# Kernel optimization log

Measured on AMD Instinct MI355X. Metric: run time of the kernel, lower is better.

The kernel has to match this reference:

```python
import jax, jax.numpy as jnp
import numpy as np

T, B, H = 1024, 16, 1024
S = 2048


def setup_inputs() -> dict:
    key = jax.random.key(0)
    k1, k2, k3, k4 = jax.random.split(key, 4)
    output = jax.random.normal(k1, (T, B, H), dtype=jnp.float32)
    memory = jax.random.normal(k2, (S, B, H), dtype=jnp.float32)
    attn_mask = jnp.zeros((B, T, S), dtype=jnp.bool_)  # True = masked
    # linear_out: Linear(2H -> H); torch weight layout [out, in]
    W = jax.random.normal(k3, (H, 2 * H), dtype=jnp.float32) * (1.0 / np.sqrt(2 * H))
    b = jax.random.normal(k4, (H,), dtype=jnp.float32) * 0.01
    return {"output": output, "memory": memory, "attn_mask": attn_mask, "W": W, "b": b}


def reference(output, memory, attn_mask, W, b):
    # scores: (B, T, S) = output^T @ memory (unscaled dot product)
    attn = jnp.einsum('tbh,sbh->bts', output, memory)
    attn = jnp.where(attn_mask, -jnp.inf, attn)
    attn = jax.nn.softmax(attn, axis=2)
    # context: (T, B, H)
    context = jnp.einsum('bts,sbh->tbh', attn, memory)
    combined = jnp.concatenate([context, output], axis=2)  # (T, B, 2H)
    out = jnp.tanh(jnp.einsum('tbd,hd->tbh', combined, W) + b)
    return (out, attn)
```

## Files before the change

kernel.cpp:

```cpp
#include <hip/hip_runtime.h>
#include <hip/hip_bf16.h>
#include <math.h>

#define Tn 1024
#define Bn 16
#define Hn 1024
#define Sn 2048

typedef __attribute__((ext_vector_type(8))) short bf16x8;
typedef __attribute__((ext_vector_type(8))) unsigned short u16x8;
typedef __attribute__((ext_vector_type(4))) float f32x4;

__device__ __forceinline__ unsigned short f2bf(float x) {
  unsigned u = __float_as_uint(x);
  u += 0x7fffu + ((u >> 16) & 1u);
  return (unsigned short)(u >> 16);
}
__device__ __forceinline__ float bf2f(unsigned short h) {
  return __uint_as_float(((unsigned)h) << 16);
}

__device__ __forceinline__ void gload16(const void* g, void* l) {
  __builtin_amdgcn_global_load_lds((const __attribute__((address_space(1))) void*)g,
                                   (__attribute__((address_space(3))) void*)l, 16, 0, 0);
}

__device__ __forceinline__ int xcd_swz(int bid, int nwg) {
  return (bid & 7) * (nwg >> 3) + (bid >> 3);
}


__global__ __launch_bounds__(256) void k_split_plane(const float* __restrict__ src,
                                                     unsigned short* __restrict__ hiP,
                                                     unsigned short* __restrict__ loP,
                                                     int rows) {
  const int i = blockIdx.x * 256 + threadIdx.x;
  const int h8 = i & (Hn / 8 - 1);
  const int rem = i >> 7;
  const int b = rem & (Bn - 1);
  const int r = rem >> 4;
  const float4 a = *(const float4*)(src + (size_t)i * 8);
  const float4 c = *(const float4*)(src + (size_t)i * 8 + 4);
  const float v[8] = {a.x, a.y, a.z, a.w, c.x, c.y, c.z, c.w};
  u16x8 hv, lv;
#pragma unroll
  for (int j = 0; j < 8; ++j) {
    const unsigned short h = f2bf(v[j]);
    hv[j] = h;
    lv[j] = f2bf(v[j] - bf2f(h));
  }
  const size_t dst = ((size_t)b * rows + r) * Hn + h8 * 8;
  *(u16x8*)(hiP + dst) = hv;
  *(u16x8*)(loP + dst) = lv;
}

__global__ __launch_bounds__(256) void k_cvt8(const float* __restrict__ src,
                                              unsigned short* __restrict__ dst, int n8) {
  const int i = blockIdx.x * 256 + threadIdx.x;
  if (i >= n8) return;
  const float4 a = *(const float4*)(src + (size_t)i * 8);
  const float4 c = *(const float4*)(src + (size_t)i * 8 + 4);
  u16x8 u;
  u[0] = f2bf(a.x); u[1] = f2bf(a.y); u[2] = f2bf(a.z); u[3] = f2bf(a.w);
  u[4] = f2bf(c.x); u[5] = f2bf(c.y); u[6] = f2bf(c.z); u[7] = f2bf(c.w);
  *(u16x8*)(dst + (size_t)i * 8) = u;
}

__global__ __launch_bounds__(256) void k_trH(const unsigned short* __restrict__ memH,
                                             unsigned short* __restrict__ memT) {
  __shared__ unsigned short L[64 * 72];
  const int t = threadIdx.x;
  const int h0 = blockIdx.x * 64, s0 = blockIdx.y * 64, b = blockIdx.z;
#pragma unroll
  for (int p = 0; p < 2; ++p) {
    const int fid = p * 256 + t;
    const int s_l = fid >> 3;
    const int c = fid & 7;
    const u16x8 v = *(const u16x8*)(memH + ((size_t)b * Sn + s0 + s_l) * Hn + h0 + c * 8);
#pragma unroll
    for (int e = 0; e < 8; ++e) L[(c * 8 + e) * 72 + s_l] = v[e];
  }
  __syncthreads();
#pragma unroll
  for (int p = 0; p < 2; ++p) {
    const int cid = p * 256 + t;
    const int h_l = cid >> 3;
    const int c = cid & 7;
    const u16x8 vv = *(const u16x8*)&L[h_l * 72 + c * 8];
    *(u16x8*)(memT + ((size_t)b * Hn + h0 + h_l) * Sn + s0 + c * 8) = vv;
  }
}


__device__ __forceinline__ void stage256x64(const unsigned short* __restrict__ g, size_t ldr,
                                            unsigned short* __restrict__ lds, int tid) {
#pragma unroll
  for (int r = 0; r < 4; ++r) {
    const int row = r * 64 + (tid >> 3);
    const int cb = (tid & 7) * 16;
    const int cs = cb ^ ((row & 4) << 3);
    gload16((const char*)g + (size_t)row * ldr * 2 + cs, (char*)lds + r * 8192 + tid * 16);
  }
}

__device__ __forceinline__ void stage256x32(const unsigned short* __restrict__ g, size_t ldr,
                                            unsigned short* __restrict__ lds, int tid) {
#pragma unroll
  for (int r = 0; r < 2; ++r) {
    const int row = r * 128 + (tid >> 2);
    const int cb = (tid & 3) * 16;
    const int cs = cb ^ ((row & 8) << 2);
    gload16((const char*)g + (size_t)row * ldr * 2 + cs, (char*)lds + r * 8192 + tid * 16);
  }
}


__global__ __launch_bounds__(512, 2) void k_scores(const unsigned short* __restrict__ oH,
                                                   const unsigned short* __restrict__ oL,
                                                   const unsigned short* __restrict__ mH,
                                                   const unsigned short* __restrict__ mL,
                                                   float* __restrict__ attn) {
  __shared__ unsigned short AsH[2][256 * 32], AsL[2][256 * 32];
  __shared__ unsigned short BsH[2][256 * 32], BsL[2][256 * 32];
  const int tid = threadIdx.x, lane = tid & 63, wv = tid >> 6;
  const int wr = wv >> 2, wc = wv & 3;
  const int swz = xcd_swz(blockIdx.x, 512);
  const int bs = (swz & 7) * 256;
  const int bt = ((swz >> 3) & 3) * 256;
  const int b = swz >> 5;
  const f32x4 fz = {0.f, 0.f, 0.f, 0.f};
  f32x4 acc[8][4];
#pragma unroll
  for (int i = 0; i < 8; ++i)
#pragma unroll
    for (int j = 0; j < 4; ++j) acc[i][j] = fz;

  const unsigned short* AgH = oH + ((size_t)b * Tn + bt) * Hn;
  const unsigned short* AgL = oL + ((size_t)b * Tn + bt) * Hn;
  const unsigned short* BgH = mH + ((size_t)b * Sn + bs) * Hn;
  const unsigned short* BgL = mL + ((size_t)b * Sn + bs) * Hn;
  const int r16 = lane & 15, khB = (lane >> 4) * 16;
  const int NK = Hn / 32;

  stage256x32(AgH, Hn, AsH[0], tid);
  stage256x32(AgL, Hn, AsL[0], tid);
  stage256x32(BgH, Hn, BsH[0], tid);
  stage256x32(BgL, Hn, BsL[0], tid);

  for (int t = 0; t < NK; ++t) {
    const int cur = t & 1;
    if (t + 1 < NK) {
      const int k0 = (t + 1) * 32;
      stage256x32(AgH + k0, Hn, AsH[cur ^ 1], tid);
      stage256x32(AgL + k0, Hn, AsL[cur ^ 1], tid);
      stage256x32(BgH + k0, Hn, BsH[cur ^ 1], tid);
      stage256x32(BgL + k0, Hn, BsL[cur ^ 1], tid);
      asm volatile("s_waitcnt vmcnt(8)" ::: "memory");
    } else {
      asm volatile("s_waitcnt vmcnt(0)" ::: "memory");
    }
    __builtin_amdgcn_s_barrier();

    const char* ABh = (const char*)AsH[cur];
    const char* ABl = (const char*)AsL[cur];
    const char* BBh = (const char*)BsH[cur];
    const char* BBl = (const char*)BsL[cur];
    bf16x8 bh[2][2], bl[2][2];
#pragma unroll
    for (int nq = 0; nq < 2; ++nq)
#pragma unroll
      for (int fj = 0; fj < 2; ++fj) {
        const int rb = wc * 64 + nq * 32 + fj * 16 + r16;
        const int off = rb * 64 + (khB ^ ((rb & 8) << 2));
        bh[nq][fj] = *(const bf16x8*)(BBh + off);
        bl[nq][fj] = *(const bf16x8*)(BBl + off);
      }
#pragma unroll
    for (int mq = 0; mq < 2; ++mq) {
      bf16x8 ah[4], al[4];
#pragma unroll
      for (int fi = 0; fi < 4; ++fi) {
        const int ra = wr * 128 + mq * 64 + fi * 16 + r16;
        const int off = ra * 64 + (khB ^ ((ra & 8) << 2));
        ah[fi] = *(const bf16x8*)(ABh + off);
        al[fi] = *(const bf16x8*)(ABl + off);
      }
      __builtin_amdgcn_s_setprio(1);
#pragma unroll
      for (int nq = 0; nq < 2; ++nq)
#pragma unroll
        for (int fj = 0; fj < 2; ++fj)
#pragma unroll
          for (int fi = 0; fi < 4; ++fi) {
            f32x4& a = acc[mq * 4 + fi][nq * 2 + fj];
            a = __builtin_amdgcn_mfma_f32_16x16x32_bf16(ah[fi], bh[nq][fj], a, 0, 0, 0);
            a = __builtin_amdgcn_mfma_f32_16x16x32_bf16(ah[fi], bl[nq][fj], a, 0, 0, 0);
            a = __builtin_amdgcn_mfma_f32_16x16x32_bf16(al[fi], bh[nq][fj], a, 0, 0, 0);
          }
      __builtin_amdgcn_s_setprio(0);
    }
    __builtin_amdgcn_s_barrier();
  }
  const int rq = (lane >> 4) * 4;
  float* obase = attn + (size_t)b * Tn * Sn;
#pragma unroll
  for (int i = 0; i < 8; ++i) {
    const int m_off = wr * 128 + (i >> 2) * 64 + (i & 3) * 16;
#pragma unroll
    for (int q = 0; q < 4; ++q) {
      const int t = bt + m_off + rq + q;
#pragma unroll
      for (int j = 0; j < 4; ++j) {
        const int s = bs + wc * 64 + (j >> 1) * 32 + (j & 1) * 16 + r16;
        obase[(size_t)t * Sn + s] = acc[i][j][q];
      }
    }
  }
}


__global__ __launch_bounds__(256) void k_softmax(float* __restrict__ attn,
                                                 const unsigned char* __restrict__ mask,
                                                 unsigned short* __restrict__ attnbf) {
  const int row = blockIdx.x;
  float* p = attn + (size_t)row * Sn;
  const unsigned char* mrow = mask + (size_t)row * Sn;
  const int tid = threadIdx.x;
  const int lane = tid & 63;
  const int wv = tid >> 6;
  const float4 a = *(const float4*)(p + tid * 8);
  const float4 c = *(const float4*)(p + tid * 8 + 4);
  const unsigned long long mv = *(const unsigned long long*)(mrow + tid * 8);
  float x[8] = {a.x, a.y, a.z, a.w, c.x, c.y, c.z, c.w};
#pragma unroll
  for (int j = 0; j < 8; ++j)
    if ((mv >> (8 * j)) & 0xffull) x[j] = -INFINITY;
  float mx = x[0];
#pragma unroll
  for (int j = 1; j < 8; ++j) mx = fmaxf(mx, x[j]);
#pragma unroll
  for (int off = 32; off; off >>= 1) mx = fmaxf(mx, __shfl_xor(mx, off, 64));
  __shared__ float redmax[4], redsum[4];
  if (lane == 0) redmax[wv] = mx;
  __syncthreads();
  mx = fmaxf(fmaxf(redmax[0], redmax[1]), fmaxf(redmax[2], redmax[3]));
  float e[8];
  float s = 0.f;
#pragma unroll
  for (int j = 0; j < 8; ++j) {
    e[j] = __expf(x[j] - mx);
    s += e[j];
  }
#pragma unroll
  for (int off = 32; off; off >>= 1) s += __shfl_xor(s, off, 64);
  if (lane == 0) redsum[wv] = s;
  __syncthreads();
  s = redsum[0] + redsum[1] + redsum[2] + redsum[3];
  const float inv = 1.0f / s;
  float o[8];
#pragma unroll
  for (int j = 0; j < 8; ++j) o[j] = e[j] * inv;
  float4 o0 = {o[0], o[1], o[2], o[3]};
  float4 o1 = {o[4], o[5], o[6], o[7]};
  *(float4*)(p + tid * 8) = o0;
  *(float4*)(p + tid * 8 + 4) = o1;
  u16x8 ub;
#pragma unroll
  for (int j = 0; j < 8; ++j) ub[j] = f2bf(o[j]);
  *(u16x8*)(attnbf + (size_t)row * Sn + tid * 8) = ub;
}


__global__ __launch_bounds__(512, 2) void k_context(const unsigned short* __restrict__ attnbf,
                                                    const unsigned short* __restrict__ memT,
                                                    unsigned short* __restrict__ ctxB) {
  __shared__ unsigned short As[2][256 * 64], Bs[2][256 * 64];
  const int tid = threadIdx.x, lane = tid & 63, wv = tid >> 6;
  const int wr = wv >> 2, wc = wv & 3;
  const int swz = xcd_swz(blockIdx.x, 256);
  const int bh = (swz & 3) * 256;
  const int bt = ((swz >> 2) & 3) * 256;
  const int b = swz >> 4;
  const f32x4 fz = {0.f, 0.f, 0.f, 0.f};
  f32x4 acc[8][4];
#pragma unroll
  for (int i = 0; i < 8; ++i)
#pragma unroll
    for (int j = 0; j < 4; ++j) acc[i][j] = fz;

  const unsigned short* Ag = attnbf + ((size_t)b * Tn + bt) * Sn;
  const unsigned short* Bg = memT + ((size_t)b * Hn + bh) * Sn;
  const int r16 = lane & 15, khB = (lane >> 4) * 16;
  const int NK = Sn / 64;

  stage256x64(Ag, Sn, As[0], tid);
  stage256x64(Bg, Sn, Bs[0], tid);

  for (int t = 0; t < NK; ++t) {
    const int cur = t & 1;
    if (t + 1 < NK) {
      const int k0 = (t + 1) * 64;
      stage256x64(Ag + k0, Sn, As[cur ^ 1], tid);
      stage256x64(Bg + k0, Sn, Bs[cur ^ 1], tid);
      asm volatile("s_waitcnt vmcnt(8)" ::: "memory");
    } else {
      asm volatile("s_waitcnt vmcnt(0)" ::: "memory");
    }
    __builtin_amdgcn_s_barrier();

    const char* Ab = (const char*)As[cur];
    const char* Bb = (const char*)Bs[cur];
    bf16x8 bb[2][2][2];
#pragma unroll
    for (int nq = 0; nq < 2; ++nq)
#pragma unroll
      for (int fj = 0; fj < 2; ++fj) {
        const int rb = wc * 64 + nq * 32 + fj * 16 + r16;
#pragma unroll
        for (int ks = 0; ks < 2; ++ks) {
          const int cb = ks * 64 + khB;
          bb[nq][fj][ks] = *(const bf16x8*)(Bb + rb * 128 + (cb ^ ((rb & 4) << 3)));
        }
      }
#pragma unroll
    for (int mq = 0; mq < 2; ++mq) {
      bf16x8 aa[4][2];
#pragma unroll
      for (int fi = 0; fi < 4; ++fi) {
        const int ra = wr * 128 + mq * 64 + fi * 16 + r16;
#pragma unroll
        for (int ks = 0; ks < 2; ++ks) {
          const int cb = ks * 64 + khB;
          aa[fi][ks] = *(const bf16x8*)(Ab + ra * 128 + (cb ^ ((ra & 4) << 3)));
        }
      }
      __builtin_amdgcn_s_setprio(1);
#pragma unroll
      for (int nq = 0; nq < 2; ++nq)
#pragma unroll
        for (int fj = 0; fj < 2; ++fj)
#pragma unroll
          for (int fi = 0; fi < 4; ++fi)
#pragma unroll
            for (int ks = 0; ks < 2; ++ks) {
              f32x4& a = acc[mq * 4 + fi][nq * 2 + fj];
              a = __builtin_amdgcn_mfma_f32_16x16x32_bf16(aa[fi][ks], bb[nq][fj][ks], a, 0, 0, 0);
            }
      __builtin_amdgcn_s_setprio(0);
    }
    __builtin_amdgcn_s_barrier();
  }
  const int rq = (lane >> 4) * 4;
#pragma unroll
  for (int i = 0; i < 8; ++i) {
    const int m_off = wr * 128 + (i >> 2) * 64 + (i & 3) * 16;
#pragma unroll
    for (int q = 0; q < 4; ++q) {
      const int t = bt + m_off + rq + q;
#pragma unroll
      for (int j = 0; j < 4; ++j) {
        const int h = bh + wc * 64 + (j >> 1) * 32 + (j & 1) * 16 + r16;
        ctxB[((size_t)b * Tn + t) * Hn + h] = f2bf(acc[i][j][q]);
      }
    }
  }
}


__global__ __launch_bounds__(512, 2) void k_final(const unsigned short* __restrict__ ctxB,
                                                  const unsigned short* __restrict__ outpH,
                                                  const unsigned short* __restrict__ Wbf,
                                                  const float* __restrict__ bias,
                                                  float* __restrict__ out) {
  __shared__ unsigned short As[2][256 * 64], Bs[2][256 * 64];
  const int tid = threadIdx.x, lane = tid & 63, wv = tid >> 6;
  const int wr = wv >> 2, wc = wv & 3;
  const int swz = xcd_swz(blockIdx.x, 256);
  const int bh = (swz & 3) * 256;
  const int bm = (swz >> 2) * 256;
  const f32x4 fz = {0.f, 0.f, 0.f, 0.f};
  f32x4 acc[8][4];
#pragma unroll
  for (int i = 0; i < 8; ++i)
#pragma unroll
    for (int j = 0; j < 4; ++j) acc[i][j] = fz;

  const int r16 = lane & 15, khB = (lane >> 4) * 16;
  const int NK = (2 * Hn) / 64;
  auto Asrc = [&](int tt) -> const unsigned short* {
    return (tt < 16) ? (ctxB + (size_t)bm * Hn + tt * 64)
                     : (outpH + (size_t)bm * Hn + (tt - 16) * 64);
  };
  const unsigned short* Bg = Wbf + (size_t)bh * (2 * Hn);

  stage256x64(Asrc(0), Hn, As[0], tid);
  stage256x64(Bg, 2 * Hn, Bs[0], tid);

  for (int t = 0; t < NK; ++t) {
    const int cur = t & 1;
    if (t + 1 < NK) {
      stage256x64(Asrc(t + 1), Hn, As[cur ^ 1], tid);
      stage256x64(Bg + (t + 1) * 64, 2 * Hn, Bs[cur ^ 1], tid);
      asm volatile("s_waitcnt vmcnt(8)" ::: "memory");
    } else {
      asm volatile("s_waitcnt vmcnt(0)" ::: "memory");
    }
    __builtin_amdgcn_s_barrier();

    const char* Ab = (const char*)As[cur];
    const char* Bb = (const char*)Bs[cur];
    bf16x8 bb[2][2][2];
#pragma unroll
    for (int nq = 0; nq < 2; ++nq)
#pragma unroll
      for (int fj = 0; fj < 2; ++fj) {
        const int rb = wc * 64 + nq * 32 + fj * 16 + r16;
#pragma unroll
        for (int ks = 0; ks < 2; ++ks) {
          const int cb = ks * 64 + khB;
          bb[nq][fj][ks] = *(const bf16x8*)(Bb + rb * 128 + (cb ^ ((rb & 4) << 3)));
        }
      }
#pragma unroll
    for (int mq = 0; mq < 2; ++mq) {
      bf16x8 aa[4][2];
#pragma unroll
      for (int fi = 0; fi < 4; ++fi) {
        const int ra = wr * 128 + mq * 64 + fi * 16 + r16;
#pragma unroll
        for (int ks = 0; ks < 2; ++ks) {
          const int cb = ks * 64 + khB;
          aa[fi][ks] = *(const bf16x8*)(Ab + ra * 128 + (cb ^ ((ra & 4) << 3)));
        }
      }
      __builtin_amdgcn_s_setprio(1);
#pragma unroll
      for (int nq = 0; nq < 2; ++nq)
#pragma unroll
        for (int fj = 0; fj < 2; ++fj)
#pragma unroll
          for (int fi = 0; fi < 4; ++fi)
#pragma unroll
            for (int ks = 0; ks < 2; ++ks) {
              f32x4& a = acc[mq * 4 + fi][nq * 2 + fj];
              a = __builtin_amdgcn_mfma_f32_16x16x32_bf16(aa[fi][ks], bb[nq][fj][ks], a, 0, 0, 0);
            }
      __builtin_amdgcn_s_setprio(0);
    }
    __builtin_amdgcn_s_barrier();
  }
  const int rq = (lane >> 4) * 4;
#pragma unroll
  for (int i = 0; i < 8; ++i) {
    const int m_off = wr * 128 + (i >> 2) * 64 + (i & 3) * 16;
#pragma unroll
    for (int q = 0; q < 4; ++q) {
      const int r = bm + m_off + rq + q;
      const int b = r >> 10, t = r & (Tn - 1);
#pragma unroll
      for (int j = 0; j < 4; ++j) {
        const int h = bh + wc * 64 + (j >> 1) * 32 + (j & 1) * 16 + r16;
        out[((size_t)t * Bn + b) * Hn + h] = tanhf(acc[i][j][q] + bias[h]);
      }
    }
  }
}

extern "C" void kernel_launch(void* const* d_in, const int* in_sizes, int n_in,
                              void* d_out, int out_size, void* d_ws, size_t ws_size,
                              hipStream_t stream) {
  const float* outp = (const float*)d_in[0];
  const float* mem = (const float*)d_in[1];
  const unsigned char* mask = (const unsigned char*)d_in[2];
  const float* W = (const float*)d_in[3];
  const float* bias = (const float*)d_in[4];
  float* out = (float*)d_out;
  float* attn = out + (size_t)Tn * Bn * Hn;

  char* w = (char*)d_ws;
  unsigned short* memH  = (unsigned short*)(w);
  unsigned short* memL  = (unsigned short*)(w + ((size_t)64 << 20));
  unsigned short* outpH = (unsigned short*)(w + ((size_t)128 << 20));
  unsigned short* outpL = (unsigned short*)(w + ((size_t)160 << 20));
  unsigned short* Wbf   = (unsigned short*)(w + ((size_t)192 << 20));
  unsigned short* memT   = memL;
  unsigned short* attnbf = memH;
  unsigned short* ctxB   = outpL;

  k_split_plane<<<dim3((Tn * Bn * Hn / 8) / 256), 256, 0, stream>>>(outp, outpH, outpL, Tn);
  k_split_plane<<<dim3((Sn * Bn * Hn / 8) / 256), 256, 0, stream>>>(mem, memH, memL, Sn);
  k_cvt8<<<dim3((Hn * 2 * Hn / 8) / 256), 256, 0, stream>>>(W, Wbf, Hn * 2 * Hn / 8);

  k_scores<<<dim3(512), 512, 0, stream>>>(outpH, outpL, memH, memL, attn);
  k_trH<<<dim3(Hn / 64, Sn / 64, Bn), 256, 0, stream>>>(memH, memT);
  k_softmax<<<dim3(Bn * Tn), 256, 0, stream>>>(attn, mask, attnbf);
  k_context<<<dim3(256), 512, 0, stream>>>(attnbf, memT, ctxB);
  k_final<<<dim3(256), 512, 0, stream>>>(ctxB, outpH, Wbf, bias, out);
}
```

Before: 533.4 us.

## Interleave prefetch stages with MFMA quadrants in scores GEMM; widen LDS swizzle

The scores kernel's K-loop now splits each iteration into four quadrant sub-steps. Each sub-step loads register fragments from LDS, issues part of the next tile's global-to-LDS prefetch, and then runs that quadrant's MFMAs, so loads are spread between compute phases instead of issued in one burst. The stage256x64 swizzle changes from a single-bit XOR to a 3-bit row XOR (row&7)<<4, matching the 128-byte rows in the other two GEMMs, to cut LDS bank conflicts. The trade-off is more barriers per iteration and a full vmcnt(0) wait at the top of each iteration.

```diff
diff --git a/kernel.cpp b/kernel.cpp
--- a/kernel.cpp
+++ b/kernel.cpp
@@ -27,6 +27,10 @@
 
 __device__ __forceinline__ int xcd_swz(int bid, int nwg) {
   return (bid & 7) * (nwg >> 3) + (bid >> 3);
+}
+
+__device__ __forceinline__ f32x4 mfma16(bf16x8 a, bf16x8 b, f32x4 c) {
+  return __builtin_amdgcn_mfma_f32_16x16x32_bf16(a, b, c, 0, 0, 0);
 }
 
 
@@ -98,7 +102,7 @@
   for (int r = 0; r < 4; ++r) {
     const int row = r * 64 + (tid >> 3);
     const int cb = (tid & 7) * 16;
-    const int cs = cb ^ ((row & 4) << 3);
+    const int cs = cb ^ ((row & 7) << 4);
     gload16((const char*)g + (size_t)row * ldr * 2 + cs, (char*)lds + r * 8192 + tid * 16);
   }
 }
@@ -149,58 +153,115 @@
 
   for (int t = 0; t < NK; ++t) {
     const int cur = t & 1;
-    if (t + 1 < NK) {
-      const int k0 = (t + 1) * 32;
-      stage256x32(AgH + k0, Hn, AsH[cur ^ 1], tid);
-      stage256x32(AgL + k0, Hn, AsL[cur ^ 1], tid);
-      stage256x32(BgH + k0, Hn, BsH[cur ^ 1], tid);
-      stage256x32(BgL + k0, Hn, BsL[cur ^ 1], tid);
-      asm volatile("s_waitcnt vmcnt(8)" ::: "memory");
-    } else {
-      asm volatile("s_waitcnt vmcnt(0)" ::: "memory");
-    }
+    asm volatile("s_waitcnt vmcnt(0)" ::: "memory");
     __builtin_amdgcn_s_barrier();
 
     const char* ABh = (const char*)AsH[cur];
     const char* ABl = (const char*)AsL[cur];
     const char* BBh = (const char*)BsH[cur];
     const char* BBl = (const char*)BsL[cur];
-    bf16x8 bh[2][2], bl[2][2];
-#pragma unroll
-    for (int nq = 0; nq < 2; ++nq)
-#pragma unroll
-      for (int fj = 0; fj < 2; ++fj) {
-        const int rb = wc * 64 + nq * 32 + fj * 16 + r16;
-        const int off = rb * 64 + (khB ^ ((rb & 8) << 2));
-        bh[nq][fj] = *(const bf16x8*)(BBh + off);
-        bl[nq][fj] = *(const bf16x8*)(BBl + off);
-      }
-#pragma unroll
-    for (int mq = 0; mq < 2; ++mq) {
-      bf16x8 ah[4], al[4];
+    const int k1 = (t + 1) * 32;
+    const bool st = (t + 1) < NK;
+
+    bf16x8 ahA[4], alA[4], bhA[2], blA[2];
+#pragma unroll
+    for (int fi = 0; fi < 4; ++fi) {
+      const int ra = wr * 128 + fi * 16 + r16;
+      const int off = ra * 64 + (khB ^ ((ra & 8) << 2));
+      ahA[fi] = *(const bf16x8*)(ABh + off);
+      alA[fi] = *(const bf16x8*)(ABl + off);
+    }
+#pragma unroll
+    for (int fj = 0; fj < 2; ++fj) {
+      const int rb = wc * 64 + fj * 16 + r16;
+      const int off = rb * 64 + (khB ^ ((rb & 8) << 2));
+      bhA[fj] = *(const bf16x8*)(BBh + off);
+      blA[fj] = *(const bf16x8*)(BBl + off);
+    }
+    if (st) {
+      stage256x32(AgH + k1, Hn, AsH[cur ^ 1], tid);
+      stage256x32(AgL + k1, Hn, AsL[cur ^ 1], tid);
+    }
+    __builtin_amdgcn_s_barrier();
+    __builtin_amdgcn_s_setprio(1);
+#pragma unroll
+    for (int fj = 0; fj < 2; ++fj)
 #pragma unroll
       for (int fi = 0; fi < 4; ++fi) {
-        const int ra = wr * 128 + mq * 64 + fi * 16 + r16;
-        const int off = ra * 64 + (khB ^ ((ra & 8) << 2));
-        ah[fi] = *(const bf16x8*)(ABh + off);
-        al[fi] = *(const bf16x8*)(ABl + off);
-      }
-      __builtin_amdgcn_s_setprio(1);
-#pragma unroll
-      for (int nq = 0; nq < 2; ++nq)
-#pragma unroll
-        for (int fj = 0; fj < 2; ++fj)
-#pragma unroll
-          for (int fi = 0; fi < 4; ++fi) {
-            f32x4& a = acc[mq * 4 + fi][nq * 2 + fj];
-            a = __builtin_amdgcn_mfma_f32_16x16x32_bf16(ah[fi], bh[nq][fj], a, 0, 0, 0);
-            a = __builtin_amdgcn_mfma_f32_16x16x32_bf16(ah[fi], bl[nq][fj], a, 0, 0, 0);
-            a = __builtin_amdgcn_mfma_f32_16x16x32_bf16(al[fi], bh[nq][fj], a, 0, 0, 0);
-          }
-      __builtin_amdgcn_s_setprio(0);
-    }
-    __builtin_amdgcn_s_barrier();
-  }
+        f32x4& a = acc[fi][fj];
+        a = mfma16(ahA[fi], bhA[fj], a);
+        a = mfma16(ahA[fi], blA[fj], a);
+        a = mfma16(alA[fi], bhA[fj], a);
+      }
+    __builtin_amdgcn_s_setprio(0);
+    __builtin_amdgcn_s_barrier();
+
+    bf16x8 ahB[4], alB[4];
+#pragma unroll
+    for (int fi = 0; fi < 4; ++fi) {
+      const int ra = wr * 128 + 64 + fi * 16 + r16;
+      const int off = ra * 64 + (khB ^ ((ra & 8) << 2));
+      ahB[fi] = *(const bf16x8*)(ABh + off);
+      alB[fi] = *(const bf16x8*)(ABl + off);
+    }
+    if (st) stage256x32(BgH + k1, Hn, BsH[cur ^ 1], tid);
+    __builtin_amdgcn_s_barrier();
+    __builtin_amdgcn_s_setprio(1);
+#pragma unroll
+    for (int fj = 0; fj < 2; ++fj)
+#pragma unroll
+      for (int fi = 0; fi < 4; ++fi) {
+        f32x4& a = acc[4 + fi][fj];
+        a = mfma16(ahB[fi], bhA[fj], a);
+        a = mfma16(ahB[fi], blA[fj], a);
+        a = mfma16(alB[fi], bhA[fj], a);
+      }
+    __builtin_amdgcn_s_setprio(0);
+    __builtin_amdgcn_s_barrier();
+
+    bf16x8 bhB[2], blB[2];
+#pragma unroll
+    for (int fj = 0; fj < 2; ++fj) {
+      const int rb = wc * 64 + 32 + fj * 16 + r16;
+      const int off = rb * 64 + (khB ^ ((rb & 8) << 2));
+      bhB[fj] = *(const bf16x8*)(BBh + off);
+      blB[fj] = *(const bf16x8*)(BBl + off);
+    }
+    if (st) stage256x32(BgL + k1, Hn, BsL[cur ^ 1], tid);
+    __builtin_amdgcn_s_barrier();
+    __builtin_amdgcn_s_setprio(1);
+#pragma unroll
+    for (int fj = 0; fj < 2; ++fj)
+#pragma unroll
+      for (int fi = 0; fi < 4; ++fi) {
+        f32x4& a = acc[4 + fi][2 + fj];
+        a = mfma16(ahB[fi], bhB[fj], a);
+        a = mfma16(ahB[fi], blB[fj], a);
+        a = mfma16(alB[fi], bhB[fj], a);
+      }
+    __builtin_amdgcn_s_setprio(0);
+    __builtin_amdgcn_s_barrier();
+
+#pragma unroll
+    for (int fi = 0; fi < 4; ++fi) {
+      const int ra = wr * 128 + fi * 16 + r16;
+      const int off = ra * 64 + (khB ^ ((ra & 8) << 2));
+      ahA[fi] = *(const bf16x8*)(ABh + off);
+      alA[fi] = *(const bf16x8*)(ABl + off);
+    }
+    __builtin_amdgcn_s_setprio(1);
+#pragma unroll
+    for (int fj = 0; fj < 2; ++fj)
+#pragma unroll
+      for (int fi = 0; fi < 4; ++fi) {
+        f32x4& a = acc[fi][2 + fj];
+        a = mfma16(ahA[fi], bhB[fj], a);
+        a = mfma16(ahA[fi], blB[fj], a);
+        a = mfma16(alA[fi], bhB[fj], a);
+      }
+    __builtin_amdgcn_s_setprio(0);
+  }
+
   const int rq = (lane >> 4) * 4;
   float* obase = attn + (size_t)b * Tn * Sn;
 #pragma unroll
@@ -319,7 +380,7 @@
 #pragma unroll
         for (int ks = 0; ks < 2; ++ks) {
           const int cb = ks * 64 + khB;
-          bb[nq][fj][ks] = *(const bf16x8*)(Bb + rb * 128 + (cb ^ ((rb & 4) << 3)));
+          bb[nq][fj][ks] = *(const bf16x8*)(Bb + rb * 128 + (cb ^ ((rb & 7) << 4)));
         }
       }
 #pragma unroll
@@ -331,7 +392,7 @@
 #pragma unroll
         for (int ks = 0; ks < 2; ++ks) {
           const int cb = ks * 64 + khB;
-          aa[fi][ks] = *(const bf16x8*)(Ab + ra * 128 + (cb ^ ((ra & 4) << 3)));
+          aa[fi][ks] = *(const bf16x8*)(Ab + ra * 128 + (cb ^ ((ra & 7) << 4)));
         }
       }
       __builtin_amdgcn_s_setprio(1);
@@ -418,7 +479,7 @@
 #pragma unroll
         for (int ks = 0; ks < 2; ++ks) {
           const int cb = ks * 64 + khB;
-          bb[nq][fj][ks] = *(const bf16x8*)(Bb + rb * 128 + (cb ^ ((rb & 4) << 3)));
+          bb[nq][fj][ks] = *(const bf16x8*)(Bb + rb * 128 + (cb ^ ((rb & 7) << 4)));
         }
       }
 #pragma unroll
@@ -430,7 +491,7 @@
 #pragma unroll
         for (int ks = 0; ks < 2; ++ks) {
           const int cb = ks * 64 + khB;
-          aa[fi][ks] = *(const bf16x8*)(Ab + ra * 128 + (cb ^ ((ra & 4) << 3)));
+          aa[fi][ks] = *(const bf16x8*)(Ab + ra * 128 + (cb ^ ((ra & 7) << 4)));
         }
       }
       __builtin_amdgcn_s_setprio(1);
```

Measured after the change: 524.3 us. Within noise of the previous version (-1.7%).

## Switch scores GEMM to 32x32 MFMA and widen LDS swizzle in 64-wide stages

Applied to the files above, without the earlier changes.

The split-bf16 scores kernel now uses 32x32x16 MFMA tiles with 16-float accumulators instead of 16x16x32, which reduces fragment loads per FLOP. The K loop now waits for all outstanding loads and barriers at the top, then issues the next prefetch. This removes the trailing barrier and the partial vmcnt overlap. Separately, the 256x64 staging and the matching reads in the two other GEMMs use a 3-bit row XOR swizzle to cut LDS bank conflicts. The risks are reduced load/compute overlap and a different output store pattern.

```diff
diff --git a/kernel.cpp b/kernel.cpp
--- a/kernel.cpp
+++ b/kernel.cpp
@@ -10,6 +10,7 @@
 typedef __attribute__((ext_vector_type(8))) short bf16x8;
 typedef __attribute__((ext_vector_type(8))) unsigned short u16x8;
 typedef __attribute__((ext_vector_type(4))) float f32x4;
+typedef __attribute__((ext_vector_type(16))) float f32x16;
 
 __device__ __forceinline__ unsigned short f2bf(float x) {
   unsigned u = __float_as_uint(x);
@@ -27,6 +28,10 @@
 
 __device__ __forceinline__ int xcd_swz(int bid, int nwg) {
   return (bid & 7) * (nwg >> 3) + (bid >> 3);
+}
+
+__device__ __forceinline__ f32x16 mfma32(bf16x8 a, bf16x8 b, f32x16 c) {
+  return __builtin_amdgcn_mfma_f32_32x32x16_bf16(a, b, c, 0, 0, 0);
 }
 
 
@@ -98,7 +103,7 @@
   for (int r = 0; r < 4; ++r) {
     const int row = r * 64 + (tid >> 3);
     const int cb = (tid & 7) * 16;
-    const int cs = cb ^ ((row & 4) << 3);
+    const int cs = cb ^ ((row & 7) << 4);
     gload16((const char*)g + (size_t)row * ldr * 2 + cs, (char*)lds + r * 8192 + tid * 16);
   }
 }
@@ -128,18 +133,20 @@
   const int bs = (swz & 7) * 256;
   const int bt = ((swz >> 3) & 3) * 256;
   const int b = swz >> 5;
-  const f32x4 fz = {0.f, 0.f, 0.f, 0.f};
-  f32x4 acc[8][4];
-#pragma unroll
-  for (int i = 0; i < 8; ++i)
-#pragma unroll
-    for (int j = 0; j < 4; ++j) acc[i][j] = fz;
+  const f32x16 fz = {0.f, 0.f, 0.f, 0.f, 0.f, 0.f, 0.f, 0.f,
+                     0.f, 0.f, 0.f, 0.f, 0.f, 0.f, 0.f, 0.f};
+  f32x16 acc[4][2];
+#pragma unroll
+  for (int i = 0; i < 4; ++i)
+#pragma unroll
+    for (int j = 0; j < 2; ++j) acc[i][j] = fz;
 
   const unsigned short* AgH = oH + ((size_t)b * Tn + bt) * Hn;
   const unsigned short* AgL = oL + ((size_t)b * Tn + bt) * Hn;
   const unsigned short* BgH = mH + ((size_t)b * Sn + bs) * Hn;
   const unsigned short* BgL = mL + ((size_t)b * Sn + bs) * Hn;
-  const int r16 = lane & 15, khB = (lane >> 4) * 16;
+  const int r32 = lane & 31;
+  const int khB = (lane >> 5) * 16;
   const int NK = Hn / 32;
 
   stage256x32(AgH, Hn, AsH[0], tid);
@@ -149,73 +156,66 @@
 
   for (int t = 0; t < NK; ++t) {
     const int cur = t & 1;
+    asm volatile("s_waitcnt vmcnt(0)" ::: "memory");
+    __builtin_amdgcn_s_barrier();
+
     if (t + 1 < NK) {
-      const int k0 = (t + 1) * 32;
-      stage256x32(AgH + k0, Hn, AsH[cur ^ 1], tid);
-      stage256x32(AgL + k0, Hn, AsL[cur ^ 1], tid);
-      stage256x32(BgH + k0, Hn, BsH[cur ^ 1], tid);
-      stage256x32(BgL + k0, Hn, BsL[cur ^ 1], tid);
-      asm volatile("s_waitcnt vmcnt(8)" ::: "memory");
-    } else {
-      asm volatile("s_waitcnt vmcnt(0)" ::: "memory");
-    }
-    __builtin_amdgcn_s_barrier();
+      const int k1 = (t + 1) * 32;
+      stage256x32(AgH + k1, Hn, AsH[cur ^ 1], tid);
+      stage256x32(AgL + k1, Hn, AsL[cur ^ 1], tid);
+      stage256x32(BgH + k1, Hn, BsH[cur ^ 1], tid);
+      stage256x32(BgL + k1, Hn, BsL[cur ^ 1], tid);
+    }
 
     const char* ABh = (const char*)AsH[cur];
     const char* ABl = (const char*)AsL[cur];
     const char* BBh = (const char*)BsH[cur];
     const char* BBl = (const char*)BsL[cur];
-    bf16x8 bh[2][2], bl[2][2];
-#pragma unroll
-    for (int nq = 0; nq < 2; ++nq)
-#pragma unroll
-      for (int fj = 0; fj < 2; ++fj) {
-        const int rb = wc * 64 + nq * 32 + fj * 16 + r16;
-        const int off = rb * 64 + (khB ^ ((rb & 8) << 2));
-        bh[nq][fj] = *(const bf16x8*)(BBh + off);
-        bl[nq][fj] = *(const bf16x8*)(BBl + off);
-      }
-#pragma unroll
-    for (int mq = 0; mq < 2; ++mq) {
-      bf16x8 ah[4], al[4];
-#pragma unroll
-      for (int fi = 0; fi < 4; ++fi) {
-        const int ra = wr * 128 + mq * 64 + fi * 16 + r16;
-        const int off = ra * 64 + (khB ^ ((ra & 8) << 2));
-        ah[fi] = *(const bf16x8*)(ABh + off);
-        al[fi] = *(const bf16x8*)(ABl + off);
-      }
-      __builtin_amdgcn_s_setprio(1);
-#pragma unroll
-      for (int nq = 0; nq < 2; ++nq)
-#pragma unroll
-        for (int fj = 0; fj < 2; ++fj)
-#pragma unroll
-          for (int fi = 0; fi < 4; ++fi) {
-            f32x4& a = acc[mq * 4 + fi][nq * 2 + fj];
-            a = __builtin_amdgcn_mfma_f32_16x16x32_bf16(ah[fi], bh[nq][fj], a, 0, 0, 0);
-            a = __builtin_amdgcn_mfma_f32_16x16x32_bf16(ah[fi], bl[nq][fj], a, 0, 0, 0);
-            a = __builtin_amdgcn_mfma_f32_16x16x32_bf16(al[fi], bh[nq][fj], a, 0, 0, 0);
-          }
-      __builtin_amdgcn_s_setprio(0);
-    }
-    __builtin_amdgcn_s_barrier();
-  }
-  const int rq = (lane >> 4) * 4;
+
+    bf16x8 ah[4][2], al[4][2];
+#pragma unroll
+    for (int fi = 0; fi < 4; ++fi)
+#pragma unroll
+      for (int ks = 0; ks < 2; ++ks) {
+        const int ra = wr * 128 + fi * 32 + r32;
+        const int off = ra * 64 + ((ks * 32 + khB) ^ ((ra & 8) << 2));
+        ah[fi][ks] = *(const bf16x8*)(ABh + off);
+        al[fi][ks] = *(const bf16x8*)(ABl + off);
+      }
+#pragma unroll
+    for (int fj = 0; fj < 2; ++fj) {
+      bf16x8 bh[2], bl[2];
+#pragma unroll
+      for (int ks = 0; ks < 2; ++ks) {
+        const int rb = wc * 64 + fj * 32 + r32;
+        const int off = rb * 64 + ((ks * 32 + khB) ^ ((rb & 8) << 2));
+        bh[ks] = *(const bf16x8*)(BBh + off);
+        bl[ks] = *(const bf16x8*)(BBl + off);
+      }
+#pragma unroll
+      for (int ks = 0; ks < 2; ++ks)
+#pragma unroll
+        for (int fi = 0; fi < 4; ++fi) {
+          acc[fi][fj] = mfma32(ah[fi][ks], bh[ks], acc[fi][fj]);
+          acc[fi][fj] = mfma32(ah[fi][ks], bl[ks], acc[fi][fj]);
+          acc[fi][fj] = mfma32(al[fi][ks], bh[ks], acc[fi][fj]);
+        }
+    }
+  }
+
+  const int roff = (lane >> 5) * 4;
   float* obase = attn + (size_t)b * Tn * Sn;
 #pragma unroll
-  for (int i = 0; i < 8; ++i) {
-    const int m_off = wr * 128 + (i >> 2) * 64 + (i & 3) * 16;
-#pragma unroll
-    for (int q = 0; q < 4; ++q) {
-      const int t = bt + m_off + rq + q;
-#pragma unroll
-      for (int j = 0; j < 4; ++j) {
-        const int s = bs + wc * 64 + (j >> 1) * 32 + (j & 1) * 16 + r16;
-        obase[(size_t)t * Sn + s] = acc[i][j][q];
-      }
-    }
-  }
+  for (int fi = 0; fi < 4; ++fi)
+#pragma unroll
+    for (int fj = 0; fj < 2; ++fj)
+#pragma unroll
+      for (int reg = 0; reg < 16; ++reg) {
+        const int row = (reg & 3) + 8 * (reg >> 2) + roff;
+        const int tt = bt + wr * 128 + fi * 32 + row;
+        const int s = bs + wc * 64 + fj * 32 + r32;
+        obase[(size_t)tt * Sn + s] = acc[fi][fj][reg];
+      }
 }
 
 
@@ -319,7 +319,7 @@
 #pragma unroll
         for (int ks = 0; ks < 2; ++ks) {
           const int cb = ks * 64 + khB;
-          bb[nq][fj][ks] = *(const bf16x8*)(Bb + rb * 128 + (cb ^ ((rb & 4) << 3)));
+          bb[nq][fj][ks] = *(const bf16x8*)(Bb + rb * 128 + (cb ^ ((rb & 7) << 4)));
         }
       }
 #pragma unroll
@@ -331,7 +331,7 @@
 #pragma unroll
         for (int ks = 0; ks < 2; ++ks) {
           const int cb = ks * 64 + khB;
-          aa[fi][ks] = *(const bf16x8*)(Ab + ra * 128 + (cb ^ ((ra & 4) << 3)));
+          aa[fi][ks] = *(const bf16x8*)(Ab + ra * 128 + (cb ^ ((ra & 7) << 4)));
         }
       }
       __builtin_amdgcn_s_setprio(1);
@@ -418,7 +418,7 @@
 #pragma unroll
         for (int ks = 0; ks < 2; ++ks) {
           const int cb = ks * 64 + khB;
-          bb[nq][fj][ks] = *(const bf16x8*)(Bb + rb * 128 + (cb ^ ((rb & 4) << 3)));
+          bb[nq][fj][ks] = *(const bf16x8*)(Bb + rb * 128 + (cb ^ ((rb & 7) << 4)));
         }
       }
 #pragma unroll
@@ -430,7 +430,7 @@
 #pragma unroll
         for (int ks = 0; ks < 2; ++ks) {
           const int cb = ks * 64 + khB;
-          aa[fi][ks] = *(const bf16x8*)(Ab + ra * 128 + (cb ^ ((ra & 4) << 3)));
+          aa[fi][ks] = *(const bf16x8*)(Ab + ra * 128 + (cb ^ ((ra & 7) << 4)));
         }
       }
       __builtin_amdgcn_s_setprio(1);
```

New measurement: 542.9 us. About the same (+1.8%).

## Interleave next-tile staging with MFMA phases and widen LDS swizzle

Applied to the files above, without the earlier changes.

The scores kernel now waits for the prior loads at the top of each iteration and issues the next A tiles before the first MFMA half and the next B tiles before the second half. This spreads global-to-LDS traffic across compute and drops one barrier per iteration. Launch bounds change from 2 to 1 blocks per CU, which frees registers but can lower occupancy. Separately, the 64-wide stage swizzle used by the context and output GEMMs now XORs on three row bits instead of one, with reads updated to match, to reduce LDS bank conflicts.

```diff
diff --git a/kernel.cpp b/kernel.cpp
--- a/kernel.cpp
+++ b/kernel.cpp
@@ -27,6 +27,10 @@
 
 __device__ __forceinline__ int xcd_swz(int bid, int nwg) {
   return (bid & 7) * (nwg >> 3) + (bid >> 3);
+}
+
+__device__ __forceinline__ f32x4 mfma16(bf16x8 a, bf16x8 b, f32x4 c) {
+  return __builtin_amdgcn_mfma_f32_16x16x32_bf16(a, b, c, 0, 0, 0);
 }
 
 
@@ -98,7 +102,7 @@
   for (int r = 0; r < 4; ++r) {
     const int row = r * 64 + (tid >> 3);
     const int cb = (tid & 7) * 16;
-    const int cs = cb ^ ((row & 4) << 3);
+    const int cs = cb ^ ((row & 7) << 4);
     gload16((const char*)g + (size_t)row * ldr * 2 + cs, (char*)lds + r * 8192 + tid * 16);
   }
 }
@@ -115,7 +119,7 @@
 }
 
 
-__global__ __launch_bounds__(512, 2) void k_scores(const unsigned short* __restrict__ oH,
+__global__ __launch_bounds__(512, 1) void k_scores(const unsigned short* __restrict__ oH,
                                                    const unsigned short* __restrict__ oL,
                                                    const unsigned short* __restrict__ mH,
                                                    const unsigned short* __restrict__ mL,
@@ -149,22 +153,21 @@
 
   for (int t = 0; t < NK; ++t) {
     const int cur = t & 1;
-    if (t + 1 < NK) {
-      const int k0 = (t + 1) * 32;
-      stage256x32(AgH + k0, Hn, AsH[cur ^ 1], tid);
-      stage256x32(AgL + k0, Hn, AsL[cur ^ 1], tid);
-      stage256x32(BgH + k0, Hn, BsH[cur ^ 1], tid);
-      stage256x32(BgL + k0, Hn, BsL[cur ^ 1], tid);
-      asm volatile("s_waitcnt vmcnt(8)" ::: "memory");
-    } else {
-      asm volatile("s_waitcnt vmcnt(0)" ::: "memory");
-    }
+    asm volatile("s_waitcnt vmcnt(0)" ::: "memory");
     __builtin_amdgcn_s_barrier();
 
+    const bool st = (t + 1) < NK;
+    const int k1 = (t + 1) * 32;
     const char* ABh = (const char*)AsH[cur];
     const char* ABl = (const char*)AsL[cur];
     const char* BBh = (const char*)BsH[cur];
     const char* BBl = (const char*)BsL[cur];
+
+    if (st) {
+      stage256x32(AgH + k1, Hn, AsH[cur ^ 1], tid);
+      stage256x32(AgL + k1, Hn, AsL[cur ^ 1], tid);
+    }
+
     bf16x8 bh[2][2], bl[2][2];
 #pragma unroll
     for (int nq = 0; nq < 2; ++nq)
@@ -175,32 +178,55 @@
         bh[nq][fj] = *(const bf16x8*)(BBh + off);
         bl[nq][fj] = *(const bf16x8*)(BBl + off);
       }
-#pragma unroll
-    for (int mq = 0; mq < 2; ++mq) {
-      bf16x8 ah[4], al[4];
-#pragma unroll
-      for (int fi = 0; fi < 4; ++fi) {
-        const int ra = wr * 128 + mq * 64 + fi * 16 + r16;
-        const int off = ra * 64 + (khB ^ ((ra & 8) << 2));
-        ah[fi] = *(const bf16x8*)(ABh + off);
-        al[fi] = *(const bf16x8*)(ABl + off);
-      }
-      __builtin_amdgcn_s_setprio(1);
-#pragma unroll
-      for (int nq = 0; nq < 2; ++nq)
-#pragma unroll
-        for (int fj = 0; fj < 2; ++fj)
-#pragma unroll
-          for (int fi = 0; fi < 4; ++fi) {
-            f32x4& a = acc[mq * 4 + fi][nq * 2 + fj];
-            a = __builtin_amdgcn_mfma_f32_16x16x32_bf16(ah[fi], bh[nq][fj], a, 0, 0, 0);
-            a = __builtin_amdgcn_mfma_f32_16x16x32_bf16(ah[fi], bl[nq][fj], a, 0, 0, 0);
-            a = __builtin_amdgcn_mfma_f32_16x16x32_bf16(al[fi], bh[nq][fj], a, 0, 0, 0);
-          }
-      __builtin_amdgcn_s_setprio(0);
-    }
-    __builtin_amdgcn_s_barrier();
-  }
+    bf16x8 ah0[4], al0[4];
+#pragma unroll
+    for (int fi = 0; fi < 4; ++fi) {
+      const int ra = wr * 128 + fi * 16 + r16;
+      const int off = ra * 64 + (khB ^ ((ra & 8) << 2));
+      ah0[fi] = *(const bf16x8*)(ABh + off);
+      al0[fi] = *(const bf16x8*)(ABl + off);
+    }
+    __builtin_amdgcn_s_setprio(1);
+#pragma unroll
+    for (int nq = 0; nq < 2; ++nq)
+#pragma unroll
+      for (int fj = 0; fj < 2; ++fj)
+#pragma unroll
+        for (int fi = 0; fi < 4; ++fi) {
+          f32x4& a = acc[fi][nq * 2 + fj];
+          a = mfma16(ah0[fi], bh[nq][fj], a);
+          a = mfma16(ah0[fi], bl[nq][fj], a);
+          a = mfma16(al0[fi], bh[nq][fj], a);
+        }
+    __builtin_amdgcn_s_setprio(0);
+
+    if (st) {
+      stage256x32(BgH + k1, Hn, BsH[cur ^ 1], tid);
+      stage256x32(BgL + k1, Hn, BsL[cur ^ 1], tid);
+    }
+    bf16x8 ah1[4], al1[4];
+#pragma unroll
+    for (int fi = 0; fi < 4; ++fi) {
+      const int ra = wr * 128 + 64 + fi * 16 + r16;
+      const int off = ra * 64 + (khB ^ ((ra & 8) << 2));
+      ah1[fi] = *(const bf16x8*)(ABh + off);
+      al1[fi] = *(const bf16x8*)(ABl + off);
+    }
+    __builtin_amdgcn_s_setprio(1);
+#pragma unroll
+    for (int nq = 0; nq < 2; ++nq)
+#pragma unroll
+      for (int fj = 0; fj < 2; ++fj)
+#pragma unroll
+        for (int fi = 0; fi < 4; ++fi) {
+          f32x4& a = acc[4 + fi][nq * 2 + fj];
+          a = mfma16(ah1[fi], bh[nq][fj], a);
+          a = mfma16(ah1[fi], bl[nq][fj], a);
+          a = mfma16(al1[fi], bh[nq][fj], a);
+        }
+    __builtin_amdgcn_s_setprio(0);
+  }
+
   const int rq = (lane >> 4) * 4;
   float* obase = attn + (size_t)b * Tn * Sn;
 #pragma unroll
@@ -319,7 +345,7 @@
 #pragma unroll
         for (int ks = 0; ks < 2; ++ks) {
           const int cb = ks * 64 + khB;
-          bb[nq][fj][ks] = *(const bf16x8*)(Bb + rb * 128 + (cb ^ ((rb & 4) << 3)));
+          bb[nq][fj][ks] = *(const bf16x8*)(Bb + rb * 128 + (cb ^ ((rb & 7) << 4)));
         }
       }
 #pragma unroll
@@ -331,7 +357,7 @@
 #pragma unroll
         for (int ks = 0; ks < 2; ++ks) {
           const int cb = ks * 64 + khB;
-          aa[fi][ks] = *(const bf16x8*)(Ab + ra * 128 + (cb ^ ((ra & 4) << 3)));
+          aa[fi][ks] = *(const bf16x8*)(Ab + ra * 128 + (cb ^ ((ra & 7) << 4)));
         }
       }
       __builtin_amdgcn_s_setprio(1);
@@ -344,7 +370,7 @@
 #pragma unroll
             for (int ks = 0; ks < 2; ++ks) {
               f32x4& a = acc[mq * 4 + fi][nq * 2 + fj];
-              a = __builtin_amdgcn_mfma_f32_16x16x32_bf16(aa[fi][ks], bb[nq][fj][ks], a, 0, 0, 0);
+              a = mfma16(aa[fi][ks], bb[nq][fj][ks], a);
             }
       __builtin_amdgcn_s_setprio(0);
     }
@@ -418,7 +444,7 @@
 #pragma unroll
         for (int ks = 0; ks < 2; ++ks) {
           const int cb = ks * 64 + khB;
-          bb[nq][fj][ks] = *(const bf16x8*)(Bb + rb * 128 + (cb ^ ((rb & 4) << 3)));
+          bb[nq][fj][ks] = *(const bf16x8*)(Bb + rb * 128 + (cb ^ ((rb & 7) << 4)));
         }
       }
 #pragma unroll
@@ -430,7 +456,7 @@
 #pragma unroll
         for (int ks = 0; ks < 2; ++ks) {
           const int cb = ks * 64 + khB;
-          aa[fi][ks] = *(const bf16x8*)(Ab + ra * 128 + (cb ^ ((ra & 4) << 3)));
+          aa[fi][ks] = *(const bf16x8*)(Ab + ra * 128 + (cb ^ ((ra & 7) << 4)));
         }
       }
       __builtin_amdgcn_s_setprio(1);
@@ -443,7 +469,7 @@
 #pragma unroll
             for (int ks = 0; ks < 2; ++ks) {
               f32x4& a = acc[mq * 4 + fi][nq * 2 + fj];
-              a = __builtin_amdgcn_mfma_f32_16x16x32_bf16(aa[fi][ks], bb[nq][fj][ks], a, 0, 0, 0);
+              a = mfma16(aa[fi][ks], bb[nq][fj][ks], a);
             }
       __builtin_amdgcn_s_setprio(0);
     }
```

New measurement: 516.0 us (median of 2 runs). 1.03x faster.
